# Kernel optimization log

Measured on AMD Instinct MI355X. Metric: run time of the kernel, lower is better.

The kernel has to match this reference:

```python
import jax, jax.numpy as jnp
import numpy as np

L = 3
NUM_NODES = 4000
NUM_RELS = 200
V = 20
EMB = 128
HID = 128
OUT = 100
N = 50000
E = 800000
B = 32
DECAY = 0.03


def setup_inputs() -> dict:
    key = jax.random.key(0)
    ks = jax.random.split(key, 20)
    s = 0.05  # weight scale
    inp = {
        'node_emb': jax.random.normal(ks[0], (NUM_NODES, EMB), jnp.float32) * s,
        'rel_emb': jax.random.normal(ks[1], (NUM_RELS, EMB), jnp.float32) * s,
        'lin_w': jax.random.normal(ks[2], (HID, EMB), jnp.float32) * s,  # torch Linear weight [out,in]
        'lin_b': jnp.zeros((HID,), jnp.float32),
        'alpha_w': jax.random.normal(ks[3], (L, NUM_NODES, NUM_NODES), jnp.float32) * 0.01,
        'alpha_b': jnp.zeros((L, NUM_NODES), jnp.float32),
        'beta_w': jax.random.normal(ks[4], (L, NUM_NODES), jnp.float32) * 0.01,
        'beta_b': jnp.zeros((L,), jnp.float32),
        'wr_w': jax.random.normal(ks[5], (L, HID), jnp.float32) * s,
        'wr_b': jnp.zeros((L,), jnp.float32),
        'conv_w': jax.random.normal(ks[6], (L, HID, HID), jnp.float32) * s,
        'conv_b': jnp.zeros((L, HID), jnp.float32),
        'mlp_w': jax.random.normal(ks[7], (OUT, 2 * HID), jnp.float32) * s,
        'mlp_b': jnp.zeros((OUT,), jnp.float32),
        'visit_node': jax.random.uniform(ks[8], (B, V, NUM_NODES), jnp.float32),
        'ehr_nodes': jax.random.uniform(ks[9], (B, NUM_NODES), jnp.float32),
        'node_ids': jax.random.randint(ks[10], (N,), 0, NUM_NODES, jnp.int32),
        'rel_ids': jax.random.randint(ks[11], (E,), 0, NUM_RELS, jnp.int32),
        'edge_index': jax.random.randint(ks[12], (2, E), 0, N, jnp.int32),
        'batch': jnp.sort(jax.random.randint(ks[13], (N,), 0, B, jnp.int32)),
    }
    return inp


def reference(node_emb, rel_emb, lin_w, lin_b, alpha_w, alpha_b, beta_w, beta_b,
              wr_w, wr_b, conv_w, conv_b, mlp_w, mlp_b, visit_node, ehr_nodes,
              node_ids, rel_ids, edge_index, batch):
    # initial node / edge features
    x = node_emb[node_ids] @ lin_w.T + lin_b                # [N, HID]
    edge_attr = rel_emb[rel_ids] @ lin_w.T + lin_b          # [E, HID]

    # temporal decay per visit: lambda_j = exp(decay*(V - j)), shape [1, V, 1]
    j = jnp.arange(V, dtype=jnp.float32)
    lam = jnp.exp(DECAY * (V - j))[None, :, None]

    src = edge_index[0]
    dst = edge_index[1]
    xj_nid = node_ids[src]                                  # [E]
    xj_bat = batch[src]                                     # [E]

    for l in range(L):
        # alpha: softmax over the visit axis (dim=1)
        alpha = jax.nn.softmax(
            jnp.einsum('bvn,mn->bvm', visit_node, alpha_w[l]) + alpha_b[l], axis=1)
        beta = jnp.tanh(
            jnp.einsum('bvn,n->bv', visit_node, beta_w[l])[:, :, None] + beta_b[l]) * lam
        attn = jnp.sum(alpha * beta, axis=1)                # [B, NUM_NODES]
        e_attn = attn[xj_bat, xj_nid][:, None]              # [E, 1]

        # BiAttentionGNNConv message + add-aggregate
        w_rel = edge_attr @ wr_w[l][:, None] + wr_b[l]      # [E, 1]
        msg = jax.nn.relu(x[src] * e_attn + w_rel * edge_attr)
        agg = jax.ops.segment_sum(msg, dst, num_segments=N)
        out = agg + x                                       # eps = 0 -> (1+eps)=1
        x = out @ conv_w[l].T + conv_b[l]                   # conv.nn Linear
        x = jax.nn.relu(x)                                  # outer F.relu (dropout inactive in eval)

    # global mean pool over graphs
    cnt = jax.ops.segment_sum(jnp.ones((N,), x.dtype), batch, num_segments=B)
    x_graph = jax.ops.segment_sum(x, batch, num_segments=B) / jnp.maximum(cnt, 1.0)[:, None]

    # patient node embedding branch
    x_node = (ehr_nodes @ node_emb) / jnp.sum(ehr_nodes, axis=1, keepdims=True)
    x_node = x_node @ lin_w.T + lin_b                       # [B, HID]

    logits = jnp.concatenate([x_graph, x_node], axis=1) @ mlp_w.T + mlp_b
    return logits
```

## Files before the change

kernel.cpp:

```cpp
#include <hip/hip_runtime.h>
#include <hip/hip_bf16.h>
#include <stdint.h>

#define LL      3
#define NNODES  4000
#define NRELS   200
#define VV      20
#define EMB     128
#define HIDD    128
#define OUTD    100
#define WS_N    50000
#define WS_E    800000
#define BV      32
#define DECAYF  0.03f

typedef __bf16 bf16x8 __attribute__((ext_vector_type(8)));
typedef __bf16 bf16x4 __attribute__((ext_vector_type(4)));
typedef __bf16 bf16x2 __attribute__((ext_vector_type(2)));
typedef float  f32x4  __attribute__((ext_vector_type(4)));

#define BM 128
#define BN 128
#define BKG 32
#define LSTR 40

template<int SPLIT>
__device__ __forceinline__ void stage_tile(const float* __restrict__ G, int rows, int Kdim,
                                           int r0, int kb, int k1, __bf16* Sh, __bf16* Sl, int tid)
{
    const int sr  = tid >> 1;
    const int skc = (tid & 1) * 16;
    const int gr  = r0 + sr;
    const int gk  = kb + skc;
    float va[16];
    if (gr < rows && gk + 16 <= k1) {
        const float4* p4 = (const float4*)(G + (long)gr * Kdim + gk);
        #pragma unroll
        for (int q = 0; q < 4; q++) {
            float4 f = p4[q];
            va[4*q+0] = f.x; va[4*q+1] = f.y; va[4*q+2] = f.z; va[4*q+3] = f.w;
        }
    } else {
        #pragma unroll
        for (int j = 0; j < 16; j++) {
            int kk = gk + j;
            va[j] = (gr < rows && kk < k1) ? G[(long)gr * Kdim + kk] : 0.0f;
        }
    }
    bf16x8 h[2], lo[2];
    #pragma unroll
    for (int half = 0; half < 2; half++) {
        #pragma unroll
        for (int j = 0; j < 8; j++) {
            float v = va[half*8 + j];
            __bf16 hi = (__bf16)v;
            h[half][j]  = hi;
            lo[half][j] = (__bf16)(v - (float)hi);
        }
    }
    *(bf16x8*)&Sh[sr*LSTR + skc]     = h[0];
    *(bf16x8*)&Sh[sr*LSTR + skc + 8] = h[1];
    if (SPLIT) {
        *(bf16x8*)&Sl[sr*LSTR + skc]     = lo[0];
        *(bf16x8*)&Sl[sr*LSTR + skc + 8] = lo[1];
    }
}

template<int SPLIT, int RELU, int BIAS, int WRITEB>
__global__ __launch_bounds__(256)
void gemm_bt(const float* __restrict__ Ag, const float* __restrict__ Bg,
             float* __restrict__ Cg, const float* __restrict__ bias,
             __bf16* __restrict__ Xb, int M, int N, int K)
{
    __shared__ __bf16 Ah[BM*LSTR];
    __shared__ __bf16 Bh[BN*LSTR];
    __shared__ __bf16 Alo[SPLIT ? BM*LSTR : 1];
    __shared__ __bf16 Blo[SPLIT ? BN*LSTR : 1];

    const int tid = threadIdx.x;
    const int m0 = blockIdx.x * BM;
    const int n0 = blockIdx.y * BN;

    const int wave = tid >> 6;
    const int lane = tid & 63;
    const int wm = (wave & 1) * 64;
    const int wn = (wave >> 1) * 64;
    const int lr = lane & 15;
    const int kq = lane >> 4;

    f32x4 acc[4][4];
    #pragma unroll
    for (int i = 0; i < 4; i++)
        #pragma unroll
        for (int j = 0; j < 4; j++)
            acc[i][j] = (f32x4){0.f, 0.f, 0.f, 0.f};

    for (int kb = 0; kb < K; kb += BKG) {
        stage_tile<SPLIT>(Ag, M, K, m0, kb, K, Ah, Alo, tid);
        stage_tile<SPLIT>(Bg, N, K, n0, kb, K, Bh, Blo, tid);
        __syncthreads();

        bf16x8 af[4], bfr[4];
        #pragma unroll
        for (int i = 0; i < 4; i++) {
            af[i]  = *(const bf16x8*)&Ah[(wm + i*16 + lr)*LSTR + kq*8];
            bfr[i] = *(const bf16x8*)&Bh[(wn + i*16 + lr)*LSTR + kq*8];
        }
        #pragma unroll
        for (int i = 0; i < 4; i++)
            #pragma unroll
            for (int j = 0; j < 4; j++)
                acc[i][j] = __builtin_amdgcn_mfma_f32_16x16x32_bf16(af[i], bfr[j], acc[i][j], 0, 0, 0);

        if (SPLIT) {
            bf16x8 al[4], bl[4];
            #pragma unroll
            for (int i = 0; i < 4; i++) {
                al[i] = *(const bf16x8*)&Alo[(wm + i*16 + lr)*LSTR + kq*8];
                bl[i] = *(const bf16x8*)&Blo[(wn + i*16 + lr)*LSTR + kq*8];
            }
            #pragma unroll
            for (int i = 0; i < 4; i++)
                #pragma unroll
                for (int j = 0; j < 4; j++) {
                    acc[i][j] = __builtin_amdgcn_mfma_f32_16x16x32_bf16(af[i], bl[j], acc[i][j], 0, 0, 0);
                    acc[i][j] = __builtin_amdgcn_mfma_f32_16x16x32_bf16(al[i], bfr[j], acc[i][j], 0, 0, 0);
                }
        }
        __syncthreads();
    }

    #pragma unroll
    for (int i = 0; i < 4; i++) {
        const int row_b = m0 + wm + i*16 + kq*4;
        #pragma unroll
        for (int j = 0; j < 4; j++) {
            const int col = n0 + wn + j*16 + lr;
            if (col < N) {
                #pragma unroll
                for (int r = 0; r < 4; r++) {
                    const int row = row_b + r;
                    if (row < M) {
                        float v = acc[i][j][r];
                        if (BIAS) v += bias[col];
                        if (RELU) v = fmaxf(v, 0.0f);
                        Cg[(long)row*N + col] = v;
                        if (WRITEB) Xb[(long)row*N + col] = (__bf16)v;
                    }
                }
            }
        }
    }
}

__global__ __launch_bounds__(256)
void gemm_alpha(const float* __restrict__ visit, const float* __restrict__ alpha_w,
                float* __restrict__ z0, float* __restrict__ z1)
{
    __shared__ __bf16 Ah[BM*LSTR];
    __shared__ __bf16 Bh[BN*LSTR];

    const int id   = blockIdx.x;
    const int xcd  = id & 7;
    const int slot = id >> 3;
    const int mi   = slot % 5;
    const int gix  = slot / 5;
    const int g    = xcd * 24 + gix;
    const int ni   = g & 31;
    const int lkh  = g >> 5;
    const int l    = lkh >> 1;
    const int kh   = lkh & 1;

    const float* Bg = alpha_w + (long)l * NNODES * NNODES;
    float*       Cg = (kh ? z1 : z0) + (long)l * (BV*VV) * NNODES;
    const int m0 = mi * BM;
    const int n0 = ni * BN;
    const int k0 = kh ? 2016 : 0;
    const int k1 = kh ? NNODES : 2016;

    const int tid = threadIdx.x;
    const int wave = tid >> 6;
    const int lane = tid & 63;
    const int wm = (wave & 1) * 64;
    const int wn = (wave >> 1) * 64;
    const int lr = lane & 15;
    const int kq = lane >> 4;

    f32x4 acc[4][4];
    #pragma unroll
    for (int i = 0; i < 4; i++)
        #pragma unroll
        for (int j = 0; j < 4; j++)
            acc[i][j] = (f32x4){0.f, 0.f, 0.f, 0.f};

    for (int kb = k0; kb < k1; kb += BKG) {
        stage_tile<0>(visit, BV*VV, NNODES, m0, kb, k1, Ah, nullptr, tid);
        stage_tile<0>(Bg, NNODES, NNODES, n0, kb, k1, Bh, nullptr, tid);
        __syncthreads();

        bf16x8 af[4], bfr[4];
        #pragma unroll
        for (int i = 0; i < 4; i++) {
            af[i]  = *(const bf16x8*)&Ah[(wm + i*16 + lr)*LSTR + kq*8];
            bfr[i] = *(const bf16x8*)&Bh[(wn + i*16 + lr)*LSTR + kq*8];
        }
        #pragma unroll
        for (int i = 0; i < 4; i++)
            #pragma unroll
            for (int j = 0; j < 4; j++)
                acc[i][j] = __builtin_amdgcn_mfma_f32_16x16x32_bf16(af[i], bfr[j], acc[i][j], 0, 0, 0);
        __syncthreads();
    }

    #pragma unroll
    for (int i = 0; i < 4; i++) {
        const int row_b = m0 + wm + i*16 + kq*4;
        #pragma unroll
        for (int j = 0; j < 4; j++) {
            const int col = n0 + wn + j*16 + lr;
            if (col < NNODES) {
                #pragma unroll
                for (int r = 0; r < 4; r++)
                    Cg[(long)(row_b + r)*NNODES + col] = acc[i][j][r];
            }
        }
    }
}

__global__ void k_count(const int* __restrict__ dst, int* __restrict__ deg) {
    int e = blockIdx.x*256 + threadIdx.x;
    if (e < WS_E) atomicAdd(&deg[dst[e]], 1);
}

__global__ __launch_bounds__(1024) void k_scan(const int* __restrict__ deg, int* __restrict__ offs,
                                               int* __restrict__ cursor, int n) {
    __shared__ int part[1024];
    int t = threadIdx.x;
    int chunk = (n + 1023) / 1024;
    int s0 = t * chunk;
    int s1 = min(s0 + chunk, n);
    int s = 0;
    for (int i = s0; i < s1; i++) s += deg[i];
    part[t] = s; __syncthreads();
    for (int off = 1; off < 1024; off <<= 1) {
        int v = part[t];
        if (t >= off) v += part[t - off];
        __syncthreads();
        part[t] = v;
        __syncthreads();
    }
    int pre = (t == 0) ? 0 : part[t - 1];
    for (int i = s0; i < s1; i++) { offs[i] = pre; cursor[i] = pre; pre += deg[i]; }
    if (t == 1023) offs[n] = pre;
}

__global__ void k_fill(const int* __restrict__ dst, const int* __restrict__ src,
                       const int* __restrict__ rel, int* __restrict__ cursor,
                       int* __restrict__ ssrc, int* __restrict__ srel) {
    int e = blockIdx.x*256 + threadIdx.x;
    if (e < WS_E) {
        int d = dst[e];
        int p = atomicAdd(&cursor[d], 1);
        ssrc[p] = src[e];
        srel[p] = rel[e];
    }
}

__global__ __launch_bounds__(128) void k_relmsg(const float* __restrict__ Wrel, const float* __restrict__ wr_w,
                                                const float* __restrict__ wr_b, __bf16* __restrict__ relmsg) {
    int l = blockIdx.x / NRELS;
    int r = blockIdx.x % NRELS;
    int o = threadIdx.x;
    float wv = Wrel[r*HIDD + o];
    __shared__ float red[128];
    red[o] = wv * wr_w[l*HIDD + o];
    __syncthreads();
    for (int s = 64; s > 0; s >>= 1) {
        if (o < s) red[o] += red[o + s];
        __syncthreads();
    }
    float wrel = red[0] + wr_b[l];
    relmsg[((long)l*NRELS + r)*HIDD + o] = (__bf16)(wrel * wv);
}

__global__ void k_xinit(const float* __restrict__ Wnode, const int* __restrict__ nid,
                        float* __restrict__ x, __bf16* __restrict__ xb) {
    int t = blockIdx.x*256 + threadIdx.x;
    if (t >= WS_N*32) return;
    int i = t >> 5;
    int d = t & 31;
    float4 v = ((const float4*)Wnode)[nid[i]*32 + d];
    ((float4*)x)[i*32 + d] = v;
    bf16x4 b;
    b[0] = (__bf16)v.x; b[1] = (__bf16)v.y; b[2] = (__bf16)v.z; b[3] = (__bf16)v.w;
    ((bf16x4*)xb)[i*32 + d] = b;
}

__global__ __launch_bounds__(256) void k_beta(const float* __restrict__ visit, const float* __restrict__ beta_w,
                                              const float* __restrict__ beta_b, float* __restrict__ beta) {
    int id = blockIdx.x;
    int l = id / (BV*VV);
    int rem = id % (BV*VV);
    int b = rem / VV;
    int v = rem % VV;
    const float* row = visit + ((long)b*VV + v) * NNODES;
    const float* wr  = beta_w + (long)l * NNODES;
    float s = 0.f;
    for (int n = threadIdx.x; n < NNODES; n += 256) s += row[n] * wr[n];
    __shared__ float red[256];
    red[threadIdx.x] = s; __syncthreads();
    for (int o = 128; o > 0; o >>= 1) {
        if (threadIdx.x < o) red[threadIdx.x] += red[threadIdx.x + o];
        __syncthreads();
    }
    if (threadIdx.x == 0) {
        float lam = __expf(DECAYF * (float)(VV - v));
        beta[id] = tanhf(red[0] + beta_b[l]) * lam;
    }
}

__global__ __launch_bounds__(256) void k_attnpool(const float* __restrict__ z0, const float* __restrict__ z1,
                                                  const float* __restrict__ beta, float* __restrict__ attn) {
    int m = blockIdx.x*256 + threadIdx.x;
    int b = blockIdx.y;
    int l = blockIdx.z;
    if (m >= NNODES) return;
    const long base = ((long)l*BV*VV + b*VV) * NNODES + m;
    const float* zb0 = z0 + base;
    const float* zb1 = z1 + base;
    const float* bet = beta + (l*BV + b) * VV;
    float zv[VV];
    float mx = -1e30f;
    #pragma unroll
    for (int v = 0; v < VV; v++) {
        zv[v] = zb0[(long)v * NNODES] + zb1[(long)v * NNODES];
        mx = fmaxf(mx, zv[v]);
    }
    float s = 0.f, ws = 0.f;
    #pragma unroll
    for (int v = 0; v < VV; v++) {
        float e = __expf(zv[v] - mx);
        s += e;
        ws += e * bet[v];
    }
    attn[((long)l*BV + b) * NNODES + m] = ws / s;
}

__global__ void k_attn_node(const float* __restrict__ attn, const int* __restrict__ batch,
                            const int* __restrict__ nid, float* __restrict__ an) {
    int i = blockIdx.x*256 + threadIdx.x;
    int l = blockIdx.y;
    if (i >= WS_N) return;
    an[(long)l*WS_N + i] = attn[((long)l*BV + batch[i]) * NNODES + nid[i]];
}

__global__ __launch_bounds__(256) void k_agg(const float* __restrict__ x, const __bf16* __restrict__ xb,
                                             const float* __restrict__ an,
                                             const __bf16* __restrict__ relmsg_l, const int* __restrict__ offs,
                                             const int* __restrict__ ssrc, const int* __restrict__ srel,
                                             float* __restrict__ outb) {
    int node = blockIdx.x*4 + (threadIdx.x >> 6);
    int lane = threadIdx.x & 63;
    if (node >= WS_N) return;
    int e0 = offs[node], e1 = offs[node + 1];
    const float2* x2  = (const float2*)x;
    const bf16x2* xb2 = (const bf16x2*)xb;
    const bf16x2* rm2 = (const bf16x2*)relmsg_l;
    float2 acc = {0.f, 0.f};
    int e = e0;
    for (; e + 3 < e1; e += 4) {
        int s0 = ssrc[e],   s1 = ssrc[e+1], s2 = ssrc[e+2], s3 = ssrc[e+3];
        int r0 = srel[e],   r1 = srel[e+1], r2 = srel[e+2], r3 = srel[e+3];
        float a0 = an[s0], a1 = an[s1], a2 = an[s2], a3 = an[s3];
        bf16x2 g0 = xb2[s0*64 + lane], g1 = xb2[s1*64 + lane];
        bf16x2 g2 = xb2[s2*64 + lane], g3 = xb2[s3*64 + lane];
        bf16x2 m0 = rm2[r0*64 + lane], m1 = rm2[r1*64 + lane];
        bf16x2 m2 = rm2[r2*64 + lane], m3 = rm2[r3*64 + lane];
        acc.x += fmaxf((float)g0[0]*a0 + (float)m0[0], 0.f) + fmaxf((float)g1[0]*a1 + (float)m1[0], 0.f)
               + fmaxf((float)g2[0]*a2 + (float)m2[0], 0.f) + fmaxf((float)g3[0]*a3 + (float)m3[0], 0.f);
        acc.y += fmaxf((float)g0[1]*a0 + (float)m0[1], 0.f) + fmaxf((float)g1[1]*a1 + (float)m1[1], 0.f)
               + fmaxf((float)g2[1]*a2 + (float)m2[1], 0.f) + fmaxf((float)g3[1]*a3 + (float)m3[1], 0.f);
    }
    for (; e < e1; e++) {
        int sa = ssrc[e], ra = srel[e];
        float aa = an[sa];
        bf16x2 ga = xb2[sa*64 + lane];
        bf16x2 va = rm2[ra*64 + lane];
        acc.x += fmaxf((float)ga[0]*aa + (float)va[0], 0.f);
        acc.y += fmaxf((float)ga[1]*aa + (float)va[1], 0.f);
    }
    float2 xo = x2[node*64 + lane];
    acc.x += xo.x; acc.y += xo.y;
    ((float2*)outb)[node*64 + lane] = acc;
}

__global__ void k_bstart(const int* __restrict__ batch, int* __restrict__ bstart) {
    int t = threadIdx.x;
    if (t > BV) return;
    int lo = 0, hi = WS_N;
    while (lo < hi) {
        int mid = (lo + hi) >> 1;
        if (batch[mid] < t) lo = mid + 1; else hi = mid;
    }
    bstart[t] = lo;
}

__global__ __launch_bounds__(256) void k_pool_partial(const float* __restrict__ x,
                                                      const int* __restrict__ batch,
                                                      float* __restrict__ xgsum) {
    int r0 = blockIdx.x * 128;
    int d = threadIdx.x & 127;
    int rofs = threadIdx.x >> 7;
    int r1 = min(r0 + 128, WS_N);
    float acc = 0.f;
    int curb = -1;
    for (int i = r0 + rofs; i < r1; i += 2) {
        int b = batch[i];
        if (b != curb) {
            if (curb >= 0) atomicAdd(&xgsum[curb*HIDD + d], acc);
            acc = 0.f; curb = b;
        }
        acc += x[(long)i*HIDD + d];
    }
    if (curb >= 0) atomicAdd(&xgsum[curb*HIDD + d], acc);
}

__global__ __launch_bounds__(128) void k_pool_fin(const float* __restrict__ xgsum,
                                                  const int* __restrict__ bstart,
                                                  float* __restrict__ xg) {
    int b = blockIdx.x;
    int d = threadIdx.x;
    int cnt = bstart[b+1] - bstart[b];
    xg[b*HIDD + d] = xgsum[b*HIDD + d] / (float)max(cnt, 1);
}

__global__ __launch_bounds__(128) void k_ehrpool(const float* __restrict__ ehr,
                                                 const float* __restrict__ node_emb,
                                                 float* __restrict__ xnsum, float* __restrict__ esum) {
    int b = blockIdx.y;
    int c = blockIdx.x;
    int d = threadIdx.x;
    int n0 = c * (NNODES/16), n1 = n0 + (NNODES/16);
    float acc = 0.f;
    for (int n = n0; n < n1; n++) {
        acc += ehr[b*NNODES + n] * node_emb[(long)n*HIDD + d];
    }
    atomicAdd(&xnsum[b*HIDD + d], acc);
    float s = 0.f;
    for (int n = n0 + d; n < n1; n += 128) s += ehr[b*NNODES + n];
    __shared__ float red[128];
    red[d] = s; __syncthreads();
    for (int o = 64; o > 0; o >>= 1) {
        if (d < o) red[d] += red[d + o];
        __syncthreads();
    }
    if (d == 0) atomicAdd(&esum[b], red[0]);
}

__global__ __launch_bounds__(128) void k_xnode_fin(const float* __restrict__ xnsum,
                                                   const float* __restrict__ esum,
                                                   const float* __restrict__ lin_w,
                                                   const float* __restrict__ lin_b,
                                                   float* __restrict__ xn) {
    int b = blockIdx.x;
    int d = threadIdx.x;
    __shared__ float t1[128];
    t1[d] = xnsum[b*HIDD + d] / esum[b];
    __syncthreads();
    float o2 = lin_b[d];
    for (int k2 = 0; k2 < HIDD; k2++) o2 += t1[k2] * lin_w[d*HIDD + k2];
    xn[b*HIDD + d] = o2;
}

__global__ __launch_bounds__(128) void k_mlp(const float* __restrict__ xg, const float* __restrict__ xn,
                                             const float* __restrict__ mlp_w, const float* __restrict__ mlp_b,
                                             float* __restrict__ out) {
    int b = blockIdx.x;
    int t = threadIdx.x;
    __shared__ float cat[2*HIDD];
    cat[t] = xg[b*HIDD + t];
    cat[HIDD + t] = xn[b*HIDD + t];
    __syncthreads();
    if (t < OUTD) {
        float acc = mlp_b[t];
        for (int j = 0; j < 2*HIDD; j++) acc += cat[j] * mlp_w[t*2*HIDD + j];
        out[b*OUTD + t] = acc;
    }
}

extern "C" void kernel_launch(void* const* d_in, const int* in_sizes, int n_in,
                              void* d_out, int out_size, void* d_ws, size_t ws_size,
                              hipStream_t stream)
{
    const float* node_emb = (const float*)d_in[0];
    const float* rel_emb  = (const float*)d_in[1];
    const float* lin_w    = (const float*)d_in[2];
    const float* lin_b    = (const float*)d_in[3];
    const float* alpha_w  = (const float*)d_in[4];
    const float* beta_w   = (const float*)d_in[6];
    const float* beta_b   = (const float*)d_in[7];
    const float* wr_w     = (const float*)d_in[8];
    const float* wr_b     = (const float*)d_in[9];
    const float* conv_w   = (const float*)d_in[10];
    const float* conv_b   = (const float*)d_in[11];
    const float* mlp_w    = (const float*)d_in[12];
    const float* mlp_b    = (const float*)d_in[13];
    const float* visit    = (const float*)d_in[14];
    const float* ehr      = (const float*)d_in[15];
    const int* node_ids   = (const int*)d_in[16];
    const int* rel_ids    = (const int*)d_in[17];
    const int* ei         = (const int*)d_in[18];
    const int* batch      = (const int*)d_in[19];
    const int* esrc = ei;
    const int* edst = ei + WS_E;
    float* out = (float*)d_out;

    char* p = (char*)d_ws;
    auto take = [&](size_t bytes) -> char* {
        char* q = p;
        p += (bytes + 255) & ~(size_t)255;
        return q;
    };
    float* x      = (float*)take((size_t)WS_N*HIDD*4);
    __bf16* xb    = (__bf16*)take((size_t)WS_N*HIDD*2);
    float* zbuf   = (float*)take((size_t)LL*BV*VV*NNODES*4);
    float* zbuf2  = (float*)take((size_t)LL*BV*VV*NNODES*4);
    float* aggbuf = zbuf;
    float* attn   = (float*)take((size_t)LL*BV*NNODES*4);
    float* betab  = (float*)take((size_t)LL*BV*VV*4);
    float* attnnd = (float*)take((size_t)LL*WS_N*4);
    float* Wnode  = (float*)take((size_t)NNODES*HIDD*4);
    float* Wrel   = (float*)take((size_t)NRELS*HIDD*4);
    __bf16* relmsg= (__bf16*)take((size_t)LL*NRELS*HIDD*2);
    float* xgsum  = (float*)take((size_t)BV*HIDD*4);
    float* xnsum  = (float*)take((size_t)BV*HIDD*4);
    float* esum   = (float*)take((size_t)BV*4);
    size_t small_zero_bytes = (size_t)((char*)(esum + BV) - (char*)xgsum);
    float* xg     = (float*)take((size_t)BV*HIDD*4);
    float* xn     = (float*)take((size_t)BV*HIDD*4);
    int* deg      = (int*)take((size_t)WS_N*4);
    int* offs     = (int*)take((size_t)(WS_N+1)*4);
    int* cursor   = (int*)take((size_t)WS_N*4);
    int* ssrc     = (int*)take((size_t)WS_E*4);
    int* srel     = (int*)take((size_t)WS_E*4);
    int* bstart   = (int*)take((size_t)(BV+1)*4);
    if ((size_t)(p - (char*)d_ws) > ws_size) return;

    (void)hipMemsetAsync(deg, 0, (size_t)WS_N*4, stream);
    (void)hipMemsetAsync(xgsum, 0, small_zero_bytes, stream);

    k_count<<<dim3((WS_E+255)/256), 256, 0, stream>>>(edst, deg);
    k_scan<<<1, 1024, 0, stream>>>(deg, offs, cursor, WS_N);
    k_fill<<<dim3((WS_E+255)/256), 256, 0, stream>>>(edst, esrc, rel_ids, cursor, ssrc, srel);

    gemm_bt<1,0,1,0><<<dim3((NNODES+BM-1)/BM, 1, 1), 256, 0, stream>>>(
        node_emb, lin_w, Wnode, lin_b, nullptr, NNODES, HIDD, HIDD);
    gemm_bt<1,0,1,0><<<dim3((NRELS+BM-1)/BM, 1, 1), 256, 0, stream>>>(
        rel_emb, lin_w, Wrel, lin_b, nullptr, NRELS, HIDD, HIDD);
    k_relmsg<<<dim3(LL*NRELS), 128, 0, stream>>>(Wrel, wr_w, wr_b, relmsg);
    k_xinit<<<dim3((WS_N*32+255)/256), 256, 0, stream>>>(Wnode, node_ids, x, xb);
    k_beta<<<dim3(LL*BV*VV), 256, 0, stream>>>(visit, beta_w, beta_b, betab);

    gemm_alpha<<<dim3(960), 256, 0, stream>>>(visit, alpha_w, zbuf, zbuf2);

    k_attnpool<<<dim3((NNODES+255)/256, BV, LL), 256, 0, stream>>>(zbuf, zbuf2, betab, attn);
    k_attn_node<<<dim3((WS_N+255)/256, LL), 256, 0, stream>>>(attn, batch, node_ids, attnnd);

    for (int l = 0; l < LL; l++) {
        k_agg<<<dim3((WS_N+3)/4), 256, 0, stream>>>(
            x, xb, attnnd + (size_t)l*WS_N, relmsg + (size_t)l*NRELS*HIDD, offs, ssrc, srel, aggbuf);
        gemm_bt<1,1,1,1><<<dim3((WS_N+BM-1)/BM, 1, 1), 256, 0, stream>>>(
            aggbuf, conv_w + (size_t)l*HIDD*HIDD, x, conv_b + (size_t)l*HIDD, xb,
            WS_N, HIDD, HIDD);
    }

    k_bstart<<<1, 64, 0, stream>>>(batch, bstart);
    k_pool_partial<<<dim3((WS_N+127)/128), 256, 0, stream>>>(x, batch, xgsum);
    k_pool_fin<<<BV, 128, 0, stream>>>(xgsum, bstart, xg);
    k_ehrpool<<<dim3(16, BV), 128, 0, stream>>>(ehr, node_emb, xnsum, esum);
    k_xnode_fin<<<BV, 128, 0, stream>>>(xnsum, esum, lin_w, lin_b, xn);
    k_mlp<<<BV, 128, 0, stream>>>(xg, xn, mlp_w, mlp_b, out);
}
```

Baseline: 952.8 us.

## Pre-convert alpha GEMM operands to bf16 and load via direct global-to-LDS

Adds a conversion kernel that casts visit_node and alpha_w to padded bf16 matrices (K padded to 4032) once per call. The alpha GEMM then streams bf16 tiles with global_load_lds into XOR-swizzled shared memory using a 64-wide K step, replacing the fp32 load-and-convert staging. The workspace is reused by aliasing graph buffers onto the bf16 alpha copy, which forces the alpha path to run before the graph setup. Separately, edge src/rel indices are packed into int2 and the aggregation loop is unrolled by 8 to raise memory-level parallelism. The conversion adds an extra full pass over the alpha weights.

New measurement: 966.6 us. No clear change (+1.4%).

```diff
diff --git a/kernel.cpp b/kernel.cpp
--- a/kernel.cpp
+++ b/kernel.cpp
@@ -13,11 +13,134 @@
 #define WS_E    800000
 #define BV      32
 #define DECAYF  0.03f
+#define AK      4032
 
 typedef __bf16 bf16x8 __attribute__((ext_vector_type(8)));
 typedef __bf16 bf16x4 __attribute__((ext_vector_type(4)));
 typedef __bf16 bf16x2 __attribute__((ext_vector_type(2)));
 typedef float  f32x4  __attribute__((ext_vector_type(4)));
+
+__device__ __forceinline__ void glds16(const __bf16* g, __bf16* l) {
+    __builtin_amdgcn_global_load_lds((const __attribute__((address_space(1))) void*)g,
+                                     (__attribute__((address_space(3))) void*)l, 16, 0, 0);
+}
+
+__global__ __launch_bounds__(256) void k_cvt(const float* __restrict__ in, __bf16* __restrict__ ob) {
+    long row = blockIdx.x;
+    const float* ip = in + row * 4000;
+    __bf16* op = ob + row * AK;
+    int t = threadIdx.x;
+    if (t < 250) {
+        const float4* p4 = (const float4*)ip + t*4;
+        float4 f0 = p4[0], f1 = p4[1], f2 = p4[2], f3 = p4[3];
+        bf16x8 h0, h1;
+        h0[0]=(__bf16)f0.x; h0[1]=(__bf16)f0.y; h0[2]=(__bf16)f0.z; h0[3]=(__bf16)f0.w;
+        h0[4]=(__bf16)f1.x; h0[5]=(__bf16)f1.y; h0[6]=(__bf16)f1.z; h0[7]=(__bf16)f1.w;
+        h1[0]=(__bf16)f2.x; h1[1]=(__bf16)f2.y; h1[2]=(__bf16)f2.z; h1[3]=(__bf16)f2.w;
+        h1[4]=(__bf16)f3.x; h1[5]=(__bf16)f3.y; h1[6]=(__bf16)f3.z; h1[7]=(__bf16)f3.w;
+        ((bf16x8*)op)[t*2]   = h0;
+        ((bf16x8*)op)[t*2+1] = h1;
+    } else if (t < 254) {
+        bf16x8 zz;
+        #pragma unroll
+        for (int j = 0; j < 8; j++) zz[j] = (__bf16)0.f;
+        ((bf16x8*)op)[500 + (t - 250)] = zz;
+    }
+}
+
+__global__ __launch_bounds__(256)
+void gemm_alpha(const __bf16* __restrict__ visit_bf, const __bf16* __restrict__ alpha_bf,
+                float* __restrict__ z0, float* __restrict__ z1)
+{
+    __shared__ __bf16 Ah[128*64];
+    __shared__ __bf16 Bh[128*64];
+
+    const int id   = blockIdx.x;
+    const int xcd  = id & 7;
+    const int slot = id >> 3;
+    const int mi   = slot % 5;
+    const int gix  = slot / 5;
+    const int g    = xcd * 24 + gix;
+    const int ni   = g & 31;
+    const int lkh  = g >> 5;
+    const int l    = lkh >> 1;
+    const int kh   = lkh & 1;
+
+    const __bf16* Ag = visit_bf;
+    const __bf16* Bg = alpha_bf + (long)l * NNODES * AK;
+    float*        Cg = (kh ? z1 : z0) + (long)l * (BV*VV) * NNODES;
+    const int m0 = mi * 128;
+    const int n0 = ni * 128;
+    const int k0 = kh ? 2048 : 0;
+    const int k1 = kh ? AK   : 2048;
+
+    const int tid = threadIdx.x;
+    const int wv  = tid >> 6;
+    const int ln  = tid & 63;
+    const int srow = ln >> 3;
+    const int gsl  = (ln & 7) ^ srow;
+
+    const __bf16* aA = Ag + (long)(m0 + wv*8 + srow) * AK + gsl*8;
+    const __bf16* bB[4];
+    #pragma unroll
+    for (int t = 0; t < 4; t++) {
+        int br = n0 + wv*8 + srow + t*32;
+        if (br > NNODES-1) br = NNODES-1;
+        bB[t] = Bg + (long)br * AK + gsl*8;
+    }
+
+    const int wm = (wv & 1) * 64;
+    const int wn = (wv >> 1) * 64;
+    const int lr = ln & 15;
+    const int kq = ln >> 4;
+    const int sw0 = lr & 7;
+
+    f32x4 acc[4][4];
+    #pragma unroll
+    for (int i = 0; i < 4; i++)
+        #pragma unroll
+        for (int j = 0; j < 4; j++)
+            acc[i][j] = (f32x4){0.f, 0.f, 0.f, 0.f};
+
+    for (int kb = k0; kb < k1; kb += 64) {
+        #pragma unroll
+        for (int t = 0; t < 4; t++) {
+            glds16(aA + (long)t*32*AK + kb, &Ah[(t*4 + wv) * 512]);
+            glds16(bB[t] + kb,              &Bh[(t*4 + wv) * 512]);
+        }
+        __syncthreads();
+        #pragma unroll
+        for (int ks = 0; ks < 2; ks++) {
+            const int sg = ((ks*4 + kq) ^ sw0) * 8;
+            bf16x8 af[4], bfr[4];
+            #pragma unroll
+            for (int i = 0; i < 4; i++) {
+                af[i]  = *(const bf16x8*)&Ah[(wm + i*16 + lr)*64 + sg];
+                bfr[i] = *(const bf16x8*)&Bh[(wn + i*16 + lr)*64 + sg];
+            }
+            #pragma unroll
+            for (int i = 0; i < 4; i++)
+                #pragma unroll
+                for (int j = 0; j < 4; j++)
+                    acc[i][j] = __builtin_amdgcn_mfma_f32_16x16x32_bf16(af[i], bfr[j], acc[i][j], 0, 0, 0);
+        }
+        __syncthreads();
+    }
+
+    #pragma unroll
+    for (int i = 0; i < 4; i++) {
+        const int row_b = m0 + wm + i*16 + kq*4;
+        #pragma unroll
+        for (int j = 0; j < 4; j++) {
+            const int col = n0 + wn + j*16 + lr;
+            if (col < NNODES) {
+                #pragma unroll
+                for (int r = 0; r < 4; r++)
+                    Cg[(long)(row_b + r)*NNODES + col] = acc[i][j][r];
+            }
+        }
+    }
+}
 
 #define BM 128
 #define BN 128
@@ -153,80 +276,6 @@
     }
 }
 
-__global__ __launch_bounds__(256)
-void gemm_alpha(const float* __restrict__ visit, const float* __restrict__ alpha_w,
-                float* __restrict__ z0, float* __restrict__ z1)
-{
-    __shared__ __bf16 Ah[BM*LSTR];
-    __shared__ __bf16 Bh[BN*LSTR];
-
-    const int id   = blockIdx.x;
-    const int xcd  = id & 7;
-    const int slot = id >> 3;
-    const int mi   = slot % 5;
-    const int gix  = slot / 5;
-    const int g    = xcd * 24 + gix;
-    const int ni   = g & 31;
-    const int lkh  = g >> 5;
-    const int l    = lkh >> 1;
-    const int kh   = lkh & 1;
-
-    const float* Bg = alpha_w + (long)l * NNODES * NNODES;
-    float*       Cg = (kh ? z1 : z0) + (long)l * (BV*VV) * NNODES;
-    const int m0 = mi * BM;
-    const int n0 = ni * BN;
-    const int k0 = kh ? 2016 : 0;
-    const int k1 = kh ? NNODES : 2016;
-
-    const int tid = threadIdx.x;
-    const int wave = tid >> 6;
-    const int lane = tid & 63;
-    const int wm = (wave & 1) * 64;
-    const int wn = (wave >> 1) * 64;
-    const int lr = lane & 15;
-    const int kq = lane >> 4;
-
-    f32x4 acc[4][4];
-    #pragma unroll
-    for (int i = 0; i < 4; i++)
-        #pragma unroll
-        for (int j = 0; j < 4; j++)
-            acc[i][j] = (f32x4){0.f, 0.f, 0.f, 0.f};
-
-    for (int kb = k0; kb < k1; kb += BKG) {
-        stage_tile<0>(visit, BV*VV, NNODES, m0, kb, k1, Ah, nullptr, tid);
-        stage_tile<0>(Bg, NNODES, NNODES, n0, kb, k1, Bh, nullptr, tid);
-        __syncthreads();
-
-        bf16x8 af[4], bfr[4];
-        #pragma unroll
-        for (int i = 0; i < 4; i++) {
-            af[i]  = *(const bf16x8*)&Ah[(wm + i*16 + lr)*LSTR + kq*8];
-            bfr[i] = *(const bf16x8*)&Bh[(wn + i*16 + lr)*LSTR + kq*8];
-        }
-        #pragma unroll
-        for (int i = 0; i < 4; i++)
-            #pragma unroll
-            for (int j = 0; j < 4; j++)
-                acc[i][j] = __builtin_amdgcn_mfma_f32_16x16x32_bf16(af[i], bfr[j], acc[i][j], 0, 0, 0);
-        __syncthreads();
-    }
-
-    #pragma unroll
-    for (int i = 0; i < 4; i++) {
-        const int row_b = m0 + wm + i*16 + kq*4;
-        #pragma unroll
-        for (int j = 0; j < 4; j++) {
-            const int col = n0 + wn + j*16 + lr;
-            if (col < NNODES) {
-                #pragma unroll
-                for (int r = 0; r < 4; r++)
-                    Cg[(long)(row_b + r)*NNODES + col] = acc[i][j][r];
-            }
-        }
-    }
-}
-
 __global__ void k_count(const int* __restrict__ dst, int* __restrict__ deg) {
     int e = blockIdx.x*256 + threadIdx.x;
     if (e < WS_E) atomicAdd(&deg[dst[e]], 1);
@@ -256,13 +305,12 @@
 
 __global__ void k_fill(const int* __restrict__ dst, const int* __restrict__ src,
                        const int* __restrict__ rel, int* __restrict__ cursor,
-                       int* __restrict__ ssrc, int* __restrict__ srel) {
+                       int2* __restrict__ sr) {
     int e = blockIdx.x*256 + threadIdx.x;
     if (e < WS_E) {
         int d = dst[e];
         int p = atomicAdd(&cursor[d], 1);
-        ssrc[p] = src[e];
-        srel[p] = rel[e];
+        sr[p] = make_int2(src[e], rel[e]);
     }
 }
 
@@ -357,39 +405,42 @@
 __global__ __launch_bounds__(256) void k_agg(const float* __restrict__ x, const __bf16* __restrict__ xb,
                                              const float* __restrict__ an,
                                              const __bf16* __restrict__ relmsg_l, const int* __restrict__ offs,
-                                             const int* __restrict__ ssrc, const int* __restrict__ srel,
+                                             const int2* __restrict__ sr,
                                              float* __restrict__ outb) {
     int node = blockIdx.x*4 + (threadIdx.x >> 6);
     int lane = threadIdx.x & 63;
     if (node >= WS_N) return;
     int e0 = offs[node], e1 = offs[node + 1];
-    const float2* x2  = (const float2*)x;
     const bf16x2* xb2 = (const bf16x2*)xb;
     const bf16x2* rm2 = (const bf16x2*)relmsg_l;
     float2 acc = {0.f, 0.f};
     int e = e0;
-    for (; e + 3 < e1; e += 4) {
-        int s0 = ssrc[e],   s1 = ssrc[e+1], s2 = ssrc[e+2], s3 = ssrc[e+3];
-        int r0 = srel[e],   r1 = srel[e+1], r2 = srel[e+2], r3 = srel[e+3];
-        float a0 = an[s0], a1 = an[s1], a2 = an[s2], a3 = an[s3];
-        bf16x2 g0 = xb2[s0*64 + lane], g1 = xb2[s1*64 + lane];
-        bf16x2 g2 = xb2[s2*64 + lane], g3 = xb2[s3*64 + lane];
-        bf16x2 m0 = rm2[r0*64 + lane], m1 = rm2[r1*64 + lane];
-        bf16x2 m2 = rm2[r2*64 + lane], m3 = rm2[r3*64 + lane];
-        acc.x += fmaxf((float)g0[0]*a0 + (float)m0[0], 0.f) + fmaxf((float)g1[0]*a1 + (float)m1[0], 0.f)
-               + fmaxf((float)g2[0]*a2 + (float)m2[0], 0.f) + fmaxf((float)g3[0]*a3 + (float)m3[0], 0.f);
-        acc.y += fmaxf((float)g0[1]*a0 + (float)m0[1], 0.f) + fmaxf((float)g1[1]*a1 + (float)m1[1], 0.f)
-               + fmaxf((float)g2[1]*a2 + (float)m2[1], 0.f) + fmaxf((float)g3[1]*a3 + (float)m3[1], 0.f);
+    for (; e + 8 <= e1; e += 8) {
+        int2 p[8];
+        #pragma unroll
+        for (int q = 0; q < 8; q++) p[q] = sr[e + q];
+        float a[8]; bf16x2 gv[8], mv[8];
+        #pragma unroll
+        for (int q = 0; q < 8; q++) a[q] = an[p[q].x];
+        #pragma unroll
+        for (int q = 0; q < 8; q++) gv[q] = xb2[p[q].x*64 + lane];
+        #pragma unroll
+        for (int q = 0; q < 8; q++) mv[q] = rm2[p[q].y*64 + lane];
+        #pragma unroll
+        for (int q = 0; q < 8; q++) {
+            acc.x += fmaxf((float)gv[q][0]*a[q] + (float)mv[q][0], 0.f);
+            acc.y += fmaxf((float)gv[q][1]*a[q] + (float)mv[q][1], 0.f);
+        }
     }
     for (; e < e1; e++) {
-        int sa = ssrc[e], ra = srel[e];
-        float aa = an[sa];
-        bf16x2 ga = xb2[sa*64 + lane];
-        bf16x2 va = rm2[ra*64 + lane];
+        int2 pa = sr[e];
+        float aa = an[pa.x];
+        bf16x2 ga = xb2[pa.x*64 + lane];
+        bf16x2 va = rm2[pa.y*64 + lane];
         acc.x += fmaxf((float)ga[0]*aa + (float)va[0], 0.f);
         acc.y += fmaxf((float)ga[1]*aa + (float)va[1], 0.f);
     }
-    float2 xo = x2[node*64 + lane];
+    float2 xo = ((const float2*)x)[node*64 + lane];
     acc.x += xo.x; acc.y += xo.y;
     ((float2*)outb)[node*64 + lane] = acc;
 }
@@ -521,17 +572,11 @@
         p += (bytes + 255) & ~(size_t)255;
         return q;
     };
-    float* x      = (float*)take((size_t)WS_N*HIDD*4);
-    __bf16* xb    = (__bf16*)take((size_t)WS_N*HIDD*2);
-    float* zbuf   = (float*)take((size_t)LL*BV*VV*NNODES*4);
-    float* zbuf2  = (float*)take((size_t)LL*BV*VV*NNODES*4);
-    float* aggbuf = zbuf;
-    float* attn   = (float*)take((size_t)LL*BV*NNODES*4);
+    float*  zbuf0    = (float*)take((size_t)LL*BV*VV*NNODES*4);
+    float*  zbuf1    = (float*)take((size_t)LL*BV*VV*NNODES*4);
+    __bf16* visit_bf = (__bf16*)take((size_t)(BV*VV)*AK*2);
+    char*   big      = take((size_t)LL*NNODES*AK*2);
     float* betab  = (float*)take((size_t)LL*BV*VV*4);
-    float* attnnd = (float*)take((size_t)LL*WS_N*4);
-    float* Wnode  = (float*)take((size_t)NNODES*HIDD*4);
-    float* Wrel   = (float*)take((size_t)NRELS*HIDD*4);
-    __bf16* relmsg= (__bf16*)take((size_t)LL*NRELS*HIDD*2);
     float* xgsum  = (float*)take((size_t)BV*HIDD*4);
     float* xnsum  = (float*)take((size_t)BV*HIDD*4);
     float* esum   = (float*)take((size_t)BV*4);
@@ -541,17 +586,38 @@
     int* deg      = (int*)take((size_t)WS_N*4);
     int* offs     = (int*)take((size_t)(WS_N+1)*4);
     int* cursor   = (int*)take((size_t)WS_N*4);
-    int* ssrc     = (int*)take((size_t)WS_E*4);
-    int* srel     = (int*)take((size_t)WS_E*4);
     int* bstart   = (int*)take((size_t)(BV+1)*4);
     if ((size_t)(p - (char*)d_ws) > ws_size) return;
 
+    __bf16* alpha_bf = (__bf16*)big;
+    char* q = big;
+    auto carve = [&](size_t bytes) -> char* {
+        char* r = q;
+        q += (bytes + 255) & ~(size_t)255;
+        return r;
+    };
+    float*  x      = (float*)carve((size_t)WS_N*HIDD*4);
+    __bf16* xb     = (__bf16*)carve((size_t)WS_N*HIDD*2);
+    int2*   sr     = (int2*)carve((size_t)WS_E*8);
+    float*  attn   = (float*)carve((size_t)LL*BV*NNODES*4);
+    float*  attnnd = (float*)carve((size_t)LL*WS_N*4);
+    float*  Wnode  = (float*)carve((size_t)NNODES*HIDD*4);
+    float*  Wrel   = (float*)carve((size_t)NRELS*HIDD*4);
+    __bf16* relmsg = (__bf16*)carve((size_t)LL*NRELS*HIDD*2);
+    float*  aggbuf = zbuf0;
+
     (void)hipMemsetAsync(deg, 0, (size_t)WS_N*4, stream);
     (void)hipMemsetAsync(xgsum, 0, small_zero_bytes, stream);
 
+    k_cvt<<<dim3(BV*VV), 256, 0, stream>>>(visit, visit_bf);
+    k_cvt<<<dim3(LL*NNODES), 256, 0, stream>>>(alpha_w, alpha_bf);
+    gemm_alpha<<<dim3(960), 256, 0, stream>>>(visit_bf, alpha_bf, zbuf0, zbuf1);
+    k_beta<<<dim3(LL*BV*VV), 256, 0, stream>>>(visit, beta_w, beta_b, betab);
+    k_attnpool<<<dim3((NNODES+255)/256, BV, LL), 256, 0, stream>>>(zbuf0, zbuf1, betab, attn);
+
     k_count<<<dim3((WS_E+255)/256), 256, 0, stream>>>(edst, deg);
     k_scan<<<1, 1024, 0, stream>>>(deg, offs, cursor, WS_N);
-    k_fill<<<dim3((WS_E+255)/256), 256, 0, stream>>>(edst, esrc, rel_ids, cursor, ssrc, srel);
+    k_fill<<<dim3((WS_E+255)/256), 256, 0, stream>>>(edst, esrc, rel_ids, cursor, sr);
 
     gemm_bt<1,0,1,0><<<dim3((NNODES+BM-1)/BM, 1, 1), 256, 0, stream>>>(
         node_emb, lin_w, Wnode, lin_b, nullptr, NNODES, HIDD, HIDD);
@@ -559,16 +625,11 @@
         rel_emb, lin_w, Wrel, lin_b, nullptr, NRELS, HIDD, HIDD);
     k_relmsg<<<dim3(LL*NRELS), 128, 0, stream>>>(Wrel, wr_w, wr_b, relmsg);
     k_xinit<<<dim3((WS_N*32+255)/256), 256, 0, stream>>>(Wnode, node_ids, x, xb);
-    k_beta<<<dim3(LL*BV*VV), 256, 0, stream>>>(visit, beta_w, beta_b, betab);
-
-    gemm_alpha<<<dim3(960), 256, 0, stream>>>(visit, alpha_w, zbuf, zbuf2);
-
-    k_attnpool<<<dim3((NNODES+255)/256, BV, LL), 256, 0, stream>>>(zbuf, zbuf2, betab, attn);
     k_attn_node<<<dim3((WS_N+255)/256, LL), 256, 0, stream>>>(attn, batch, node_ids, attnnd);
 
     for (int l = 0; l < LL; l++) {
         k_agg<<<dim3((WS_N+3)/4), 256, 0, stream>>>(
-            x, xb, attnnd + (size_t)l*WS_N, relmsg + (size_t)l*NRELS*HIDD, offs, ssrc, srel, aggbuf);
+            x, xb, attnnd + (size_t)l*WS_N, relmsg + (size_t)l*NRELS*HIDD, offs, sr, aggbuf);
         gemm_bt<1,1,1,1><<<dim3((WS_N+BM-1)/BM, 1, 1), 256, 0, stream>>>(
             aggbuf, conv_w + (size_t)l*HIDD*HIDD, x, conv_b + (size_t)l*HIDD, xb,
             WS_N, HIDD, HIDD);
```
